# Performance work log

Hardware: AMD Instinct MI355X
Metric: run time of the kernel (lower is better)

## Reference

```python
import jax, jax.numpy as jnp
import numpy as np

EPS = 1e-12

def _l2norm(v):
    return v / (jnp.linalg.norm(v) + EPS)

def _spectral_norm_weight(W, u):
    # torch spectral_norm with n_power_iterations=1: v = norm(W^T u); u' = norm(W v);
    # sigma = u'^T W v with u', v detached; returns W / sigma.
    v = jax.lax.stop_gradient(_l2norm(W.T @ u))
    u2 = jax.lax.stop_gradient(_l2norm(W @ v))
    sigma = u2 @ (W @ v)
    return W / sigma

def setup_inputs() -> dict:
    key = jax.random.key(0)
    ks = jax.random.split(key, 8)
    C, H, W = 64, 96, 96
    Cfg = C // 8
    g = 1e-2  # small weight scale (module uses orthogonal init with tiny gain)
    return {
        "x":  jax.random.normal(ks[0], (1, C, H, W), jnp.float32),
        "Wf": jax.random.normal(ks[1], (Cfg, C), jnp.float32) * g,
        "bf": jnp.zeros((Cfg,), jnp.float32),
        "Wg": jax.random.normal(ks[2], (Cfg, C), jnp.float32) * g,
        "bg": jnp.zeros((Cfg,), jnp.float32),
        "Wh": jax.random.normal(ks[3], (C, C), jnp.float32) * g,
        "bh": jnp.zeros((C,), jnp.float32),
        "gamma": jax.random.normal(ks[4], (1,), jnp.float32),
        "uf": jax.random.normal(ks[5], (Cfg,), jnp.float32),
        "ug": jax.random.normal(ks[6], (Cfg,), jnp.float32),
        "uh": jax.random.normal(ks[7], (C,), jnp.float32),
    }

def reference(x, Wf, bf, Wg, bg, Wh, bh, gamma, uf, ug, uh):
    B, C, H, Wd = x.shape
    N = H * Wd
    xf = x.reshape(B, C, N)  # 1x1 convs act per-pixel -> matmul over channel dim
    Wf_sn = _spectral_norm_weight(Wf, uf)
    Wg_sn = _spectral_norm_weight(Wg, ug)
    Wh_sn = _spectral_norm_weight(Wh, uh)
    f_flat = jnp.einsum('oc,bcn->bon', Wf_sn, xf) + bf[:, None]  # [B,Cfg,N]
    g_flat = jnp.einsum('oc,bcn->bon', Wg_sn, xf) + bg[:, None]  # [B,Cfg,N]
    h_flat = jnp.einsum('oc,bcn->bon', Wh_sn, xf) + bh[:, None]  # [B,C,N]
    # s[b,n,m] = sum_k g[b,k,n] * f[b,k,m]  (g^T f)
    s = jnp.einsum('bkn,bkm->bnm', g_flat, f_flat)  # [B,N,N]
    beta = jax.nn.softmax(s, axis=1)                # softmax over dim=1 (g axis)
    o = jnp.einsum('bcn,bnm->bcm', h_flat, beta)    # [B,C,N]
    o = o.reshape(B, C, H, Wd)
    return gamma * o + x
```

## Files before the change

kernel.cpp:

```cpp
#include <hip/hip_runtime.h>
#include <hip/hip_bf16.h>

#define NPIX 9216
#define MTILES (NPIX / 16)

typedef __attribute__((ext_vector_type(4))) float f32x4;
typedef __attribute__((ext_vector_type(8))) short bf16x8;
typedef __attribute__((ext_vector_type(2))) unsigned int u32x2;

__device__ __forceinline__ void gload_lds16(const void* g, void* l) {
  __builtin_amdgcn_global_load_lds(
      (const __attribute__((address_space(1))) unsigned int*)g,
      (__attribute__((address_space(3))) unsigned int*)l, 16, 0, 0);
}
__device__ __forceinline__ void gload_lds4(const void* g, void* l) {
  __builtin_amdgcn_global_load_lds(
      (const __attribute__((address_space(1))) unsigned int*)g,
      (__attribute__((address_space(3))) unsigned int*)l, 4, 0, 0);
}
#define LDS_OFF(p) ((unsigned)(unsigned long long)(const __attribute__((address_space(3))) char*)(const char*)(p))

__global__ __launch_bounds__(256) void spectral_kernel(
    const float* __restrict__ Wf, const float* __restrict__ bfv,
    const float* __restrict__ Wg, const float* __restrict__ bgv,
    const float* __restrict__ Wh, const float* __restrict__ bhv,
    const float* __restrict__ uf, const float* __restrict__ ug,
    const float* __restrict__ uh,
    float* __restrict__ Wsc, float* __restrict__ bsc) {
  __shared__ float vsh3[3][64];
  __shared__ float is_s[3];
  const int tid = threadIdx.x;
  const int wv = tid >> 6, t = tid & 63;
  if (wv < 3) {
    const float* W = (wv == 0) ? Wf : (wv == 1) ? Wg : Wh;
    const float* u = (wv == 0) ? uf : (wv == 1) ? ug : uh;
    const int O = (wv == 2) ? 64 : 8;
    float v = 0.f;
    for (int o = 0; o < O; ++o) v += W[o * 64 + t] * u[o];
    float s = v * v;
    for (int off = 32; off; off >>= 1) s += __shfl_xor(s, off);
    vsh3[wv][t] = v / (sqrtf(s) + 1e-12f);
    float wvv = 0.f;
    if (t < O) { for (int c = 0; c < 64; ++c) wvv += W[t * 64 + c] * vsh3[wv][c]; }
    float s2 = (t < O) ? wvv * wvv : 0.f;
    for (int off = 32; off; off >>= 1) s2 += __shfl_xor(s2, off);
    const float nw = sqrtf(s2);
    if (t == 0) is_s[wv] = (nw + 1e-12f) / s2;
  }
  __syncthreads();
  const float sf = is_s[0] * 0.25f, sg = is_s[1], sh = is_s[2];
  for (int e = tid; e < 5120; e += 256) {
    const int r = e >> 6, c = e & 63;
    float val;
    if (r < 8)       val = Wf[r * 64 + c] * sf;
    else if (r < 16) val = Wg[(r - 8) * 64 + c] * sg;
    else             val = Wh[(r - 16) * 64 + c] * sh;
    Wsc[e] = val;
  }
  if (tid < 80) {
    bsc[tid] = (tid < 8) ? bfv[tid] * 0.25f
             : (tid < 16) ? bgv[tid - 8] : bhv[tid - 16];
  }
}

__global__ __launch_bounds__(256) void fgh_kernel(
    const float* __restrict__ x,
    const float* __restrict__ Wsc, const float* __restrict__ bsc,
    ushort* __restrict__ Qp, ushort* __restrict__ Kp, ushort* __restrict__ Vt2) {
  const int tid = threadIdx.x;
  const int px = tid & 63;
  const int rw = __builtin_amdgcn_readfirstlane(tid >> 6);
  const int r0 = blockIdx.y * 16 + rw * 4;
  const int p  = blockIdx.x * 64 + px;

  float xv[64];
  #pragma unroll
  for (int c = 0; c < 64; ++c) xv[c] = x[c * NPIX + p];

  float acc0 = 0.f, acc1 = 0.f, acc2 = 0.f, acc3 = 0.f;
  const float* w0 = Wsc + (r0 + 0) * 64;
  const float* w1 = Wsc + (r0 + 1) * 64;
  const float* w2 = Wsc + (r0 + 2) * 64;
  const float* w3 = Wsc + (r0 + 3) * 64;
  #pragma unroll
  for (int c = 0; c < 64; ++c) {
    const float xc = xv[c];
    acc0 += w0[c] * xc; acc1 += w1[c] * xc;
    acc2 += w2[c] * xc; acc3 += w3[c] * xc;
  }

  const int tile = p >> 5, nt = p & 31;
  const int tt = nt >> 4, gg = (nt >> 2) & 3, ii = nt & 3;
  const int kbase = tile * 512 + nt * 8;
  float accs[4] = {acc0, acc1, acc2, acc3};
  #pragma unroll
  for (int j = 0; j < 4; ++j) {
    const int r = r0 + j;
    const float val = accs[j] + bsc[r];
    if (r < 8) {
      const __hip_bfloat16 h = __float2bfloat16(val);
      const float hf = __bfloat162float(h);
      const __hip_bfloat16 lo = __float2bfloat16(val - hf);
      Qp[p * 16 + r]     = *(const ushort*)&h;
      Qp[p * 16 + 8 + r] = *(const ushort*)&lo;
    } else if (r < 16) {
      const int rk = r - 8;
      const __hip_bfloat16 h = __float2bfloat16(val);
      const float hf = __bfloat162float(h);
      const __hip_bfloat16 lo = __float2bfloat16(val - hf);
      Kp[kbase + rk]       = *(const ushort*)&h;
      Kp[kbase + 256 + rk] = *(const ushort*)&lo;
    } else {
      const int rv = r - 16;
      const __hip_bfloat16 hv = __float2bfloat16(val);
      const int idx = tile * 2048 +
          ((rv * 32 + gg * 8 + tt * 4 + ii) ^ (((rv >> 1) & 7) << 3));
      Vt2[idx] = *(const ushort*)&hv;
    }
  }
}

template <int S>
__global__ __launch_bounds__(256) void attn_kernel(
    const ushort* __restrict__ Qp, const ushort* __restrict__ Kp,
    const ushort* __restrict__ Vt2,
    ushort* __restrict__ Om,
    float* __restrict__ Sm) {
  constexpr int NSEG = NPIX / S;
  constexpr int NT = NSEG / 32;
  __shared__ ushort Vs[4][2048];
  __shared__ ushort Ks[4][512];
  const int tid  = threadIdx.x;
  const int w    = tid >> 6;
  const int l    = tid & 63;
  const int mloc = l & 15;
  const int g    = l >> 4;
  const int spl  = blockIdx.y;
  const int mrow = blockIdx.x * 64 + w * 16 + mloc;

  bf16x8 qh = *(const bf16x8*)(Qp + mrow * 16);
  bf16x8 ql = *(const bf16x8*)(Qp + mrow * 16 + 8);
  asm volatile("" : "+v"(qh), "+v"(ql));

  const int n0 = spl * NSEG;
  const char* vsrc = (const char*)Vt2 + ((size_t)(n0 >> 5)) * 4096 + w * 1024 + l * 16;
  const char* ksrc = (const char*)Kp + ((size_t)(n0 >> 5)) * 1024 + w * 256 + l * 4;

  #define STAGE(t_) do {                                                  \
    const int b_ = (t_) & 3;                                              \
    gload_lds16(vsrc + (size_t)(t_) * 4096, (char*)&Vs[b_][0] + w * 1024);\
    gload_lds4 (ksrc + (size_t)(t_) * 1024, (char*)&Ks[b_][0] + w * 256); \
  } while (0)

  STAGE(0);
  STAGE(1);

  const unsigned ks_base = LDS_OFF(&Ks[0][0]);
  const unsigned vs_base = LDS_OFF(&Vs[0][0]);
  const unsigned vswz = (mloc * 64 + g * 16) ^ (((mloc >> 1) & 7) << 4);

  float mx = -INFINITY, ls = 0.f;
  const f32x4 zero = {0.f, 0.f, 0.f, 0.f};
  f32x4 acc0 = zero, acc1 = zero, acc2 = zero, acc3 = zero;

  for (int t = 0; t < NT; ++t) {
    const int b = t & 3;
    if (t + 2 < NT) {
      STAGE(t + 2);
      asm volatile("s_waitcnt vmcnt(4)" ::: "memory");
    } else if (t + 1 < NT) {
      asm volatile("s_waitcnt vmcnt(2)" ::: "memory");
    } else {
      asm volatile("s_waitcnt vmcnt(0)" ::: "memory");
    }
    __builtin_amdgcn_s_barrier();

    const unsigned kaddr = ks_base + b * 1024 + mloc * 16;
    const unsigned vaddr = vs_base + b * 4096 + vswz;
    bf16x8 kh0, kl0, kh1, kl1, v0, v1, v2, v3;
    asm volatile("ds_read_b128 %0, %1"            : "=v"(kh0) : "v"(kaddr));
    asm volatile("ds_read_b128 %0, %1 offset:256" : "=v"(kh1) : "v"(kaddr));
    asm volatile("ds_read_b128 %0, %1 offset:512" : "=v"(kl0) : "v"(kaddr));
    asm volatile("ds_read_b128 %0, %1 offset:768" : "=v"(kl1) : "v"(kaddr));
    asm volatile("ds_read_b128 %0, %1"            : "=v"(v0)  : "v"(vaddr));
    asm volatile("ds_read_b128 %0, %1 offset:1024": "=v"(v1)  : "v"(vaddr));
    asm volatile("ds_read_b128 %0, %1 offset:2048": "=v"(v2)  : "v"(vaddr));
    asm volatile("ds_read_b128 %0, %1 offset:3072": "=v"(v3)  : "v"(vaddr));
    asm volatile("s_waitcnt lgkmcnt(0)" ::: "memory");
    __builtin_amdgcn_sched_barrier(0);

    f32x4 s0 = zero, s1 = zero;
    s0 = __builtin_amdgcn_mfma_f32_16x16x32_bf16(kh0, qh, s0, 0, 0, 0);
    s1 = __builtin_amdgcn_mfma_f32_16x16x32_bf16(kh1, qh, s1, 0, 0, 0);
    s0 = __builtin_amdgcn_mfma_f32_16x16x32_bf16(kh0, ql, s0, 0, 0, 0);
    s1 = __builtin_amdgcn_mfma_f32_16x16x32_bf16(kh1, ql, s1, 0, 0, 0);
    s0 = __builtin_amdgcn_mfma_f32_16x16x32_bf16(kl0, qh, s0, 0, 0, 0);
    s1 = __builtin_amdgcn_mfma_f32_16x16x32_bf16(kl1, qh, s1, 0, 0, 0);

    const float tm = fmaxf(
        fmaxf(fmaxf(s0[0], s0[1]), fmaxf(s0[2], s0[3])),
        fmaxf(fmaxf(s1[0], s1[1]), fmaxf(s1[2], s1[3])));
    if (__any(tm > mx + 8.0f)) {
      float tr = fmaxf(tm, __shfl_xor(tm, 16));
      tr = fmaxf(tr, __shfl_xor(tr, 32));
      const float mxn = fmaxf(mx, tr);
      const float corr = __expf(mx - mxn);
      ls *= corr;
      const float c0 = __shfl(corr, (g << 2) + 0);
      const float c1 = __shfl(corr, (g << 2) + 1);
      const float c2 = __shfl(corr, (g << 2) + 2);
      const float c3 = __shfl(corr, (g << 2) + 3);
      acc0[0] *= c0; acc0[1] *= c1; acc0[2] *= c2; acc0[3] *= c3;
      acc1[0] *= c0; acc1[1] *= c1; acc1[2] *= c2; acc1[3] *= c3;
      acc2[0] *= c0; acc2[1] *= c1; acc2[2] *= c2; acc2[3] *= c3;
      acc3[0] *= c0; acc3[1] *= c1; acc3[2] *= c2; acc3[3] *= c3;
      mx = mxn;
    }
    float pj[8];
    pj[0] = __expf(s0[0] - mx); pj[1] = __expf(s0[1] - mx);
    pj[2] = __expf(s0[2] - mx); pj[3] = __expf(s0[3] - mx);
    pj[4] = __expf(s1[0] - mx); pj[5] = __expf(s1[1] - mx);
    pj[6] = __expf(s1[2] - mx); pj[7] = __expf(s1[3] - mx);
    ls += ((pj[0] + pj[1]) + (pj[2] + pj[3])) + ((pj[4] + pj[5]) + (pj[6] + pj[7]));

    union { unsigned int u[4]; bf16x8 v; } pu;
    #pragma unroll
    for (int jj = 0; jj < 4; ++jj) {
      unsigned int r;
      asm("v_cvt_pk_bf16_f32 %0, %1, %2" : "=v"(r) : "v"(pj[2 * jj]), "v"(pj[2 * jj + 1]));
      pu.u[jj] = r;
    }
    acc0 = __builtin_amdgcn_mfma_f32_16x16x32_bf16(pu.v, v0, acc0, 0, 0, 0);
    acc1 = __builtin_amdgcn_mfma_f32_16x16x32_bf16(pu.v, v1, acc1, 0, 0, 0);
    acc2 = __builtin_amdgcn_mfma_f32_16x16x32_bf16(pu.v, v2, acc2, 0, 0, 0);
    acc3 = __builtin_amdgcn_mfma_f32_16x16x32_bf16(pu.v, v3, acc3, 0, 0, 0);
  }
  #undef STAGE

  ls += __shfl_xor(ls, 16);
  ls += __shfl_xor(ls, 32);

  const size_t mt = (size_t)blockIdx.x * 4 + w;
  ushort* Ob = Om + (mt * S + spl) * 1024;
  float*  Sb = Sm + (mt * S + spl) * 32;
  #pragma unroll
  for (int ct = 0; ct < 4; ++ct) {
    const f32x4 a = (ct == 0) ? acc0 : (ct == 1) ? acc1 : (ct == 2) ? acc2 : acc3;
    unsigned int r0, r1;
    asm("v_cvt_pk_bf16_f32 %0, %1, %2" : "=v"(r0) : "v"(a[0]), "v"(a[1]));
    asm("v_cvt_pk_bf16_f32 %0, %1, %2" : "=v"(r1) : "v"(a[2]), "v"(a[3]));
    u32x2 pk; pk[0] = r0; pk[1] = r1;
    *(u32x2*)(Ob + (ct * 16 + mloc) * 16 + 4 * g) = pk;
  }
  if (l < 16) { Sb[l] = mx; Sb[16 + l] = ls; }
}

template <int S>
__global__ __launch_bounds__(256) void combine_kernel(
    const ushort* __restrict__ Om, const float* __restrict__ Sm,
    const float* __restrict__ x, const float* __restrict__ gammap,
    float* __restrict__ out) {
  const int mt = blockIdx.x;
  const int m0 = mt * 16;
  const float gamma = gammap[0];
  const float* Sb = Sm + (size_t)mt * S * 32;
  const ushort* Ob = Om + (size_t)mt * S * 1024;
  for (int e = threadIdx.x; e < 1024; e += 256) {
    const int m = e & 15, c = e >> 4;
    float M = -INFINITY;
    #pragma unroll
    for (int s = 0; s < S; ++s) M = fmaxf(M, Sb[s * 32 + m]);
    float L = 0.f, val = 0.f;
    #pragma unroll
    for (int s = 0; s < S; ++s) {
      const float wgt = __expf(Sb[s * 32 + m] - M);
      L += Sb[s * 32 + 16 + m] * wgt;
      union { unsigned int i; float f; } cv;
      cv.i = ((unsigned int)Ob[s * 1024 + e]) << 16;
      val += cv.f * wgt;
    }
    const int idx = c * NPIX + m0 + m;
    out[idx] = gamma * (val / L) + x[idx];
  }
}

extern "C" void kernel_launch(void* const* d_in, const int* in_sizes, int n_in,
                              void* d_out, int out_size, void* d_ws, size_t ws_size,
                              hipStream_t stream) {
  const float* x     = (const float*)d_in[0];
  const float* Wf    = (const float*)d_in[1];
  const float* bf    = (const float*)d_in[2];
  const float* Wg    = (const float*)d_in[3];
  const float* bg    = (const float*)d_in[4];
  const float* Wh    = (const float*)d_in[5];
  const float* bh    = (const float*)d_in[6];
  const float* gamma = (const float*)d_in[7];
  const float* uf    = (const float*)d_in[8];
  const float* ug    = (const float*)d_in[9];
  const float* uh    = (const float*)d_in[10];
  float* out = (float*)d_out;

  char* ws = (char*)d_ws;
  float*  Wsc = (float*)(ws);
  float*  bsc = (float*)(ws + 20480);
  ushort* Qp  = (ushort*)(ws + 21504);
  ushort* Kp  = (ushort*)(ws + 21504 + NPIX * 16 * 2);
  ushort* Vt2 = (ushort*)(ws + 21504 + 2 * NPIX * 16 * 2);
  const size_t off = 21504 + (size_t)2 * NPIX * 16 * 2 + (size_t)NPIX * 64 * 2;
  ushort* Om = (ushort*)(ws + off);
  const size_t need16 = off + (size_t)MTILES * 16 * 1024 * 2 + (size_t)MTILES * 16 * 32 * 4;

  spectral_kernel<<<1, 256, 0, stream>>>(Wf, bf, Wg, bg, Wh, bh, uf, ug, uh, Wsc, bsc);
  fgh_kernel<<<dim3(NPIX / 64, 5), 256, 0, stream>>>(x, Wsc, bsc, Qp, Kp, Vt2);
  if (ws_size >= need16) {
    float* Sm = (float*)(ws + off + (size_t)MTILES * 16 * 1024 * 2);
    attn_kernel<16><<<dim3(NPIX / 64, 16), 256, 0, stream>>>(Qp, Kp, Vt2, Om, Sm);
    combine_kernel<16><<<MTILES, 256, 0, stream>>>(Om, Sm, x, gamma, out);
  } else {
    float* Sm = (float*)(ws + off + (size_t)MTILES * 8 * 1024 * 2);
    attn_kernel<8><<<dim3(NPIX / 64, 8), 256, 0, stream>>>(Qp, Kp, Vt2, Om, Sm);
    combine_kernel<8><<<MTILES, 256, 0, stream>>>(Om, Sm, x, gamma, out);
  }
}
```

Baseline: 77.60 us.

## Restructure attention pipeline: 2-wave blocks, triple buffering, exp2 softmax, split 8

Attention blocks shrink from four waves to two, covering 32 query rows, and the KV split is fixed at 8, so the grid becomes 288x8 with 128 threads per block. Staging moves from a 4-deep to a 3-deep LDS ring and is issued after the barrier, using only 16-byte global-to-LDS loads. The log2(e) factor is folded into the f-projection weights and bias so every softmax exp becomes exp2f, with the rescale threshold adjusted to match. The V LDS reads are waited on only just before the PV MFMAs, letting them overlap the QK MFMAs and exponentials. Fewer waves per block and more blocks change occupancy and per-block LDS reuse, and the fallback path for small workspaces is removed.

```diff
diff --git a/kernel.cpp b/kernel.cpp
--- a/kernel.cpp
+++ b/kernel.cpp
@@ -3,6 +3,7 @@
 
 #define NPIX 9216
 #define MTILES (NPIX / 16)
+#define SPLIT 8
 
 typedef __attribute__((ext_vector_type(4))) float f32x4;
 typedef __attribute__((ext_vector_type(8))) short bf16x8;
@@ -12,11 +13,6 @@
   __builtin_amdgcn_global_load_lds(
       (const __attribute__((address_space(1))) unsigned int*)g,
       (__attribute__((address_space(3))) unsigned int*)l, 16, 0, 0);
-}
-__device__ __forceinline__ void gload_lds4(const void* g, void* l) {
-  __builtin_amdgcn_global_load_lds(
-      (const __attribute__((address_space(1))) unsigned int*)g,
-      (__attribute__((address_space(3))) unsigned int*)l, 4, 0, 0);
 }
 #define LDS_OFF(p) ((unsigned)(unsigned long long)(const __attribute__((address_space(3))) char*)(const char*)(p))
 
@@ -48,7 +44,8 @@
     if (t == 0) is_s[wv] = (nw + 1e-12f) / s2;
   }
   __syncthreads();
-  const float sf = is_s[0] * 0.25f, sg = is_s[1], sh = is_s[2];
+  const float LOG2E = 1.44269504f;
+  const float sf = is_s[0] * 0.25f * LOG2E, sg = is_s[1], sh = is_s[2];
   for (int e = tid; e < 5120; e += 256) {
     const int r = e >> 6, c = e & 63;
     float val;
@@ -58,7 +55,7 @@
     Wsc[e] = val;
   }
   if (tid < 80) {
-    bsc[tid] = (tid < 8) ? bfv[tid] * 0.25f
+    bsc[tid] = (tid < 8) ? bfv[tid] * 0.25f * LOG2E
              : (tid < 16) ? bgv[tid - 8] : bhv[tid - 16];
   }
 }
@@ -121,35 +118,36 @@
 }
 
 template <int S>
-__global__ __launch_bounds__(256) void attn_kernel(
+__global__ __launch_bounds__(128) void attn_kernel(
     const ushort* __restrict__ Qp, const ushort* __restrict__ Kp,
     const ushort* __restrict__ Vt2,
     ushort* __restrict__ Om,
     float* __restrict__ Sm) {
   constexpr int NSEG = NPIX / S;
   constexpr int NT = NSEG / 32;
-  __shared__ ushort Vs[4][2048];
-  __shared__ ushort Ks[4][512];
+  __shared__ ushort Vs[3][2048];
+  __shared__ ushort Ks[3][512];
   const int tid  = threadIdx.x;
   const int w    = tid >> 6;
   const int l    = tid & 63;
   const int mloc = l & 15;
   const int g    = l >> 4;
   const int spl  = blockIdx.y;
-  const int mrow = blockIdx.x * 64 + w * 16 + mloc;
+  const int mrow = blockIdx.x * 32 + w * 16 + mloc;
 
   bf16x8 qh = *(const bf16x8*)(Qp + mrow * 16);
   bf16x8 ql = *(const bf16x8*)(Qp + mrow * 16 + 8);
   asm volatile("" : "+v"(qh), "+v"(ql));
 
   const int n0 = spl * NSEG;
-  const char* vsrc = (const char*)Vt2 + ((size_t)(n0 >> 5)) * 4096 + w * 1024 + l * 16;
-  const char* ksrc = (const char*)Kp + ((size_t)(n0 >> 5)) * 1024 + w * 256 + l * 4;
-
-  #define STAGE(t_) do {                                                  \
-    const int b_ = (t_) & 3;                                              \
-    gload_lds16(vsrc + (size_t)(t_) * 4096, (char*)&Vs[b_][0] + w * 1024);\
-    gload_lds4 (ksrc + (size_t)(t_) * 1024, (char*)&Ks[b_][0] + w * 256); \
+  const char* vsrc = (const char*)Vt2 + ((size_t)(n0 >> 5)) * 4096 + w * 2048 + l * 16;
+  const char* ksrc = (const char*)Kp + ((size_t)(n0 >> 5)) * 1024 + l * 16;
+
+  #define STAGE(t_) do {                                                      \
+    const int b_ = (t_) % 3;                                                  \
+    gload_lds16(vsrc + (size_t)(t_) * 4096,        (char*)&Vs[b_][0] + w * 2048);        \
+    gload_lds16(vsrc + (size_t)(t_) * 4096 + 1024, (char*)&Vs[b_][0] + w * 2048 + 1024); \
+    gload_lds16(ksrc + (size_t)(t_) * 1024,        (char*)&Ks[b_][0]);        \
   } while (0)
 
   STAGE(0);
@@ -163,17 +161,16 @@
   const f32x4 zero = {0.f, 0.f, 0.f, 0.f};
   f32x4 acc0 = zero, acc1 = zero, acc2 = zero, acc3 = zero;
 
+  #pragma unroll 6
   for (int t = 0; t < NT; ++t) {
-    const int b = t & 3;
-    if (t + 2 < NT) {
-      STAGE(t + 2);
-      asm volatile("s_waitcnt vmcnt(4)" ::: "memory");
-    } else if (t + 1 < NT) {
-      asm volatile("s_waitcnt vmcnt(2)" ::: "memory");
+    const int b = t % 3;
+    if (t + 1 < NT) {
+      asm volatile("s_waitcnt vmcnt(3)" ::: "memory");
     } else {
       asm volatile("s_waitcnt vmcnt(0)" ::: "memory");
     }
     __builtin_amdgcn_s_barrier();
+    if (t + 2 < NT) STAGE(t + 2);
 
     const unsigned kaddr = ks_base + b * 1024 + mloc * 16;
     const unsigned vaddr = vs_base + b * 4096 + vswz;
@@ -186,7 +183,7 @@
     asm volatile("ds_read_b128 %0, %1 offset:1024": "=v"(v1)  : "v"(vaddr));
     asm volatile("ds_read_b128 %0, %1 offset:2048": "=v"(v2)  : "v"(vaddr));
     asm volatile("ds_read_b128 %0, %1 offset:3072": "=v"(v3)  : "v"(vaddr));
-    asm volatile("s_waitcnt lgkmcnt(0)" ::: "memory");
+    asm volatile("s_waitcnt lgkmcnt(4)" ::: "memory");
     __builtin_amdgcn_sched_barrier(0);
 
     f32x4 s0 = zero, s1 = zero;
@@ -197,14 +194,15 @@
     s0 = __builtin_amdgcn_mfma_f32_16x16x32_bf16(kl0, qh, s0, 0, 0, 0);
     s1 = __builtin_amdgcn_mfma_f32_16x16x32_bf16(kl1, qh, s1, 0, 0, 0);
 
-    const float tm = fmaxf(
-        fmaxf(fmaxf(s0[0], s0[1]), fmaxf(s0[2], s0[3])),
-        fmaxf(fmaxf(s1[0], s1[1]), fmaxf(s1[2], s1[3])));
-    if (__any(tm > mx + 8.0f)) {
+    const float m1 = fmaxf(fmaxf(s0[0], s0[1]), s0[2]);
+    const float m2 = fmaxf(fmaxf(s0[3], s1[0]), s1[1]);
+    const float m3 = fmaxf(fmaxf(s1[2], s1[3]), m1);
+    const float tm = fmaxf(m2, m3);
+    if (__any(tm > mx + 11.5416f)) {
       float tr = fmaxf(tm, __shfl_xor(tm, 16));
       tr = fmaxf(tr, __shfl_xor(tr, 32));
       const float mxn = fmaxf(mx, tr);
-      const float corr = __expf(mx - mxn);
+      const float corr = exp2f(mx - mxn);
       ls *= corr;
       const float c0 = __shfl(corr, (g << 2) + 0);
       const float c1 = __shfl(corr, (g << 2) + 1);
@@ -217,10 +215,10 @@
       mx = mxn;
     }
     float pj[8];
-    pj[0] = __expf(s0[0] - mx); pj[1] = __expf(s0[1] - mx);
-    pj[2] = __expf(s0[2] - mx); pj[3] = __expf(s0[3] - mx);
-    pj[4] = __expf(s1[0] - mx); pj[5] = __expf(s1[1] - mx);
-    pj[6] = __expf(s1[2] - mx); pj[7] = __expf(s1[3] - mx);
+    pj[0] = exp2f(s0[0] - mx); pj[1] = exp2f(s0[1] - mx);
+    pj[2] = exp2f(s0[2] - mx); pj[3] = exp2f(s0[3] - mx);
+    pj[4] = exp2f(s1[0] - mx); pj[5] = exp2f(s1[1] - mx);
+    pj[6] = exp2f(s1[2] - mx); pj[7] = exp2f(s1[3] - mx);
     ls += ((pj[0] + pj[1]) + (pj[2] + pj[3])) + ((pj[4] + pj[5]) + (pj[6] + pj[7]));
 
     union { unsigned int u[4]; bf16x8 v; } pu;
@@ -230,6 +228,8 @@
       asm("v_cvt_pk_bf16_f32 %0, %1, %2" : "=v"(r) : "v"(pj[2 * jj]), "v"(pj[2 * jj + 1]));
       pu.u[jj] = r;
     }
+    asm volatile("s_waitcnt lgkmcnt(0)" ::: "memory");
+    __builtin_amdgcn_sched_barrier(0);
     acc0 = __builtin_amdgcn_mfma_f32_16x16x32_bf16(pu.v, v0, acc0, 0, 0, 0);
     acc1 = __builtin_amdgcn_mfma_f32_16x16x32_bf16(pu.v, v1, acc1, 0, 0, 0);
     acc2 = __builtin_amdgcn_mfma_f32_16x16x32_bf16(pu.v, v2, acc2, 0, 0, 0);
@@ -240,7 +240,7 @@
   ls += __shfl_xor(ls, 16);
   ls += __shfl_xor(ls, 32);
 
-  const size_t mt = (size_t)blockIdx.x * 4 + w;
+  const size_t mt = (size_t)blockIdx.x * 2 + w;
   ushort* Ob = Om + (mt * S + spl) * 1024;
   float*  Sb = Sm + (mt * S + spl) * 32;
   #pragma unroll
@@ -273,7 +273,7 @@
     float L = 0.f, val = 0.f;
     #pragma unroll
     for (int s = 0; s < S; ++s) {
-      const float wgt = __expf(Sb[s * 32 + m] - M);
+      const float wgt = exp2f(Sb[s * 32 + m] - M);
       L += Sb[s * 32 + 16 + m] * wgt;
       union { unsigned int i; float f; } cv;
       cv.i = ((unsigned int)Ob[s * 1024 + e]) << 16;
@@ -308,17 +308,10 @@
   ushort* Vt2 = (ushort*)(ws + 21504 + 2 * NPIX * 16 * 2);
   const size_t off = 21504 + (size_t)2 * NPIX * 16 * 2 + (size_t)NPIX * 64 * 2;
   ushort* Om = (ushort*)(ws + off);
-  const size_t need16 = off + (size_t)MTILES * 16 * 1024 * 2 + (size_t)MTILES * 16 * 32 * 4;
+  float*  Sm = (float*)(ws + off + (size_t)MTILES * SPLIT * 1024 * 2);
 
   spectral_kernel<<<1, 256, 0, stream>>>(Wf, bf, Wg, bg, Wh, bh, uf, ug, uh, Wsc, bsc);
   fgh_kernel<<<dim3(NPIX / 64, 5), 256, 0, stream>>>(x, Wsc, bsc, Qp, Kp, Vt2);
-  if (ws_size >= need16) {
-    float* Sm = (float*)(ws + off + (size_t)MTILES * 16 * 1024 * 2);
-    attn_kernel<16><<<dim3(NPIX / 64, 16), 256, 0, stream>>>(Qp, Kp, Vt2, Om, Sm);
-    combine_kernel<16><<<MTILES, 256, 0, stream>>>(Om, Sm, x, gamma, out);
-  } else {
-    float* Sm = (float*)(ws + off + (size_t)MTILES * 8 * 1024 * 2);
-    attn_kernel<8><<<dim3(NPIX / 64, 8), 256, 0, stream>>>(Qp, Kp, Vt2, Om, Sm);
-    combine_kernel<8><<<MTILES, 256, 0, stream>>>(Om, Sm, x, gamma, out);
-  }
-}
+  attn_kernel<SPLIT><<<dim3(NPIX / 32, SPLIT), 128, 0, stream>>>(Qp, Kp, Vt2, Om, Sm);
+  combine_kernel<SPLIT><<<MTILES, 256, 0, stream>>>(Om, Sm, x, gamma, out);
+}
```

Result: slower. 83.02 us (+7.0%).

## Process two query tiles per wave, fold log2e into Q, split combine blocks

Applied to the files above, without the earlier changes.

Each attention wave now handles two 16-row query tiles, so every K/V tile staged in LDS is reused twice and the grid is halved. QK MFMAs start after a partial LDS wait, overlapping with the V reads. Log2(e) is folded into the f weights and bias so the softmax can use exp2f, with the rescale threshold adjusted to match. The combine kernel is split into four blocks per tile for more parallelism. The cost is roughly double the accumulator registers, which may lower occupancy, plus fewer attention blocks.

```diff
diff --git a/kernel.cpp b/kernel.cpp
--- a/kernel.cpp
+++ b/kernel.cpp
@@ -48,7 +48,8 @@
     if (t == 0) is_s[wv] = (nw + 1e-12f) / s2;
   }
   __syncthreads();
-  const float sf = is_s[0] * 0.25f, sg = is_s[1], sh = is_s[2];
+  const float LOG2E = 1.44269504f;
+  const float sf = is_s[0] * 0.25f * LOG2E, sg = is_s[1], sh = is_s[2];
   for (int e = tid; e < 5120; e += 256) {
     const int r = e >> 6, c = e & 63;
     float val;
@@ -58,7 +59,7 @@
     Wsc[e] = val;
   }
   if (tid < 80) {
-    bsc[tid] = (tid < 8) ? bfv[tid] * 0.25f
+    bsc[tid] = (tid < 8) ? bfv[tid] * 0.25f * LOG2E
              : (tid < 16) ? bgv[tid - 8] : bhv[tid - 16];
   }
 }
@@ -120,6 +121,45 @@
   }
 }
 
+__device__ __forceinline__ void softmax_step(
+    const f32x4 s0, const f32x4 s1, int g, float& mx, float& ls,
+    f32x4& a0, f32x4& a1, f32x4& a2, f32x4& a3, bf16x8& pv) {
+  const float m1 = fmaxf(fmaxf(s0[0], s0[1]), s0[2]);
+  const float m2 = fmaxf(fmaxf(s0[3], s1[0]), s1[1]);
+  const float m3 = fmaxf(fmaxf(s1[2], s1[3]), m1);
+  const float tm = fmaxf(m2, m3);
+  if (__any(tm > mx + 11.5416f)) {
+    float tr = fmaxf(tm, __shfl_xor(tm, 16));
+    tr = fmaxf(tr, __shfl_xor(tr, 32));
+    const float mxn = fmaxf(mx, tr);
+    const float corr = exp2f(mx - mxn);
+    ls *= corr;
+    const float c0 = __shfl(corr, (g << 2) + 0);
+    const float c1 = __shfl(corr, (g << 2) + 1);
+    const float c2 = __shfl(corr, (g << 2) + 2);
+    const float c3 = __shfl(corr, (g << 2) + 3);
+    a0[0] *= c0; a0[1] *= c1; a0[2] *= c2; a0[3] *= c3;
+    a1[0] *= c0; a1[1] *= c1; a1[2] *= c2; a1[3] *= c3;
+    a2[0] *= c0; a2[1] *= c1; a2[2] *= c2; a2[3] *= c3;
+    a3[0] *= c0; a3[1] *= c1; a3[2] *= c2; a3[3] *= c3;
+    mx = mxn;
+  }
+  float pj[8];
+  pj[0] = exp2f(s0[0] - mx); pj[1] = exp2f(s0[1] - mx);
+  pj[2] = exp2f(s0[2] - mx); pj[3] = exp2f(s0[3] - mx);
+  pj[4] = exp2f(s1[0] - mx); pj[5] = exp2f(s1[1] - mx);
+  pj[6] = exp2f(s1[2] - mx); pj[7] = exp2f(s1[3] - mx);
+  ls += ((pj[0] + pj[1]) + (pj[2] + pj[3])) + ((pj[4] + pj[5]) + (pj[6] + pj[7]));
+  union { unsigned int u[4]; bf16x8 v; } pu;
+  #pragma unroll
+  for (int jj = 0; jj < 4; ++jj) {
+    unsigned int r;
+    asm("v_cvt_pk_bf16_f32 %0, %1, %2" : "=v"(r) : "v"(pj[2 * jj]), "v"(pj[2 * jj + 1]));
+    pu.u[jj] = r;
+  }
+  pv = pu.v;
+}
+
 template <int S>
 __global__ __launch_bounds__(256) void attn_kernel(
     const ushort* __restrict__ Qp, const ushort* __restrict__ Kp,
@@ -136,11 +176,14 @@
   const int mloc = l & 15;
   const int g    = l >> 4;
   const int spl  = blockIdx.y;
-  const int mrow = blockIdx.x * 64 + w * 16 + mloc;
-
-  bf16x8 qh = *(const bf16x8*)(Qp + mrow * 16);
-  bf16x8 ql = *(const bf16x8*)(Qp + mrow * 16 + 8);
-  asm volatile("" : "+v"(qh), "+v"(ql));
+  const int mrow0 = blockIdx.x * 128 + w * 32 + mloc;
+  const int mrow1 = mrow0 + 16;
+
+  bf16x8 qh0 = *(const bf16x8*)(Qp + mrow0 * 16);
+  bf16x8 ql0 = *(const bf16x8*)(Qp + mrow0 * 16 + 8);
+  bf16x8 qh1 = *(const bf16x8*)(Qp + mrow1 * 16);
+  bf16x8 ql1 = *(const bf16x8*)(Qp + mrow1 * 16 + 8);
+  asm volatile("" : "+v"(qh0), "+v"(ql0), "+v"(qh1), "+v"(ql1));
 
   const int n0 = spl * NSEG;
   const char* vsrc = (const char*)Vt2 + ((size_t)(n0 >> 5)) * 4096 + w * 1024 + l * 16;
@@ -159,9 +202,10 @@
   const unsigned vs_base = LDS_OFF(&Vs[0][0]);
   const unsigned vswz = (mloc * 64 + g * 16) ^ (((mloc >> 1) & 7) << 4);
 
-  float mx = -INFINITY, ls = 0.f;
+  float mx0 = -INFINITY, ls0 = 0.f, mx1 = -INFINITY, ls1 = 0.f;
   const f32x4 zero = {0.f, 0.f, 0.f, 0.f};
-  f32x4 acc0 = zero, acc1 = zero, acc2 = zero, acc3 = zero;
+  f32x4 p0a0 = zero, p0a1 = zero, p0a2 = zero, p0a3 = zero;
+  f32x4 p1a0 = zero, p1a1 = zero, p1a2 = zero, p1a3 = zero;
 
   for (int t = 0; t < NT; ++t) {
     const int b = t & 3;
@@ -186,73 +230,66 @@
     asm volatile("ds_read_b128 %0, %1 offset:1024": "=v"(v1)  : "v"(vaddr));
     asm volatile("ds_read_b128 %0, %1 offset:2048": "=v"(v2)  : "v"(vaddr));
     asm volatile("ds_read_b128 %0, %1 offset:3072": "=v"(v3)  : "v"(vaddr));
+    asm volatile("s_waitcnt lgkmcnt(4)" ::: "memory");
+    __builtin_amdgcn_sched_barrier(0);
+
+    f32x4 s00 = zero, s01 = zero, s10 = zero, s11 = zero;
+    s00 = __builtin_amdgcn_mfma_f32_16x16x32_bf16(kh0, qh0, s00, 0, 0, 0);
+    s01 = __builtin_amdgcn_mfma_f32_16x16x32_bf16(kh1, qh0, s01, 0, 0, 0);
+    s10 = __builtin_amdgcn_mfma_f32_16x16x32_bf16(kh0, qh1, s10, 0, 0, 0);
+    s11 = __builtin_amdgcn_mfma_f32_16x16x32_bf16(kh1, qh1, s11, 0, 0, 0);
+    s00 = __builtin_amdgcn_mfma_f32_16x16x32_bf16(kh0, ql0, s00, 0, 0, 0);
+    s01 = __builtin_amdgcn_mfma_f32_16x16x32_bf16(kh1, ql0, s01, 0, 0, 0);
+    s10 = __builtin_amdgcn_mfma_f32_16x16x32_bf16(kh0, ql1, s10, 0, 0, 0);
+    s11 = __builtin_amdgcn_mfma_f32_16x16x32_bf16(kh1, ql1, s11, 0, 0, 0);
+    s00 = __builtin_amdgcn_mfma_f32_16x16x32_bf16(kl0, qh0, s00, 0, 0, 0);
+    s01 = __builtin_amdgcn_mfma_f32_16x16x32_bf16(kl1, qh0, s01, 0, 0, 0);
+    s10 = __builtin_amdgcn_mfma_f32_16x16x32_bf16(kl0, qh1, s10, 0, 0, 0);
+    s11 = __builtin_amdgcn_mfma_f32_16x16x32_bf16(kl1, qh1, s11, 0, 0, 0);
+
+    bf16x8 pv0, pv1;
+    softmax_step(s00, s01, g, mx0, ls0, p0a0, p0a1, p0a2, p0a3, pv0);
+    softmax_step(s10, s11, g, mx1, ls1, p1a0, p1a1, p1a2, p1a3, pv1);
+
     asm volatile("s_waitcnt lgkmcnt(0)" ::: "memory");
     __builtin_amdgcn_sched_barrier(0);
-
-    f32x4 s0 = zero, s1 = zero;
-    s0 = __builtin_amdgcn_mfma_f32_16x16x32_bf16(kh0, qh, s0, 0, 0, 0);
-    s1 = __builtin_amdgcn_mfma_f32_16x16x32_bf16(kh1, qh, s1, 0, 0, 0);
-    s0 = __builtin_amdgcn_mfma_f32_16x16x32_bf16(kh0, ql, s0, 0, 0, 0);
-    s1 = __builtin_amdgcn_mfma_f32_16x16x32_bf16(kh1, ql, s1, 0, 0, 0);
-    s0 = __builtin_amdgcn_mfma_f32_16x16x32_bf16(kl0, qh, s0, 0, 0, 0);
-    s1 = __builtin_amdgcn_mfma_f32_16x16x32_bf16(kl1, qh, s1, 0, 0, 0);
-
-    const float tm = fmaxf(
-        fmaxf(fmaxf(s0[0], s0[1]), fmaxf(s0[2], s0[3])),
-        fmaxf(fmaxf(s1[0], s1[1]), fmaxf(s1[2], s1[3])));
-    if (__any(tm > mx + 8.0f)) {
-      float tr = fmaxf(tm, __shfl_xor(tm, 16));
-      tr = fmaxf(tr, __shfl_xor(tr, 32));
-      const float mxn = fmaxf(mx, tr);
-      const float corr = __expf(mx - mxn);
-      ls *= corr;
-      const float c0 = __shfl(corr, (g << 2) + 0);
-      const float c1 = __shfl(corr, (g << 2) + 1);
-      const float c2 = __shfl(corr, (g << 2) + 2);
-      const float c3 = __shfl(corr, (g << 2) + 3);
-      acc0[0] *= c0; acc0[1] *= c1; acc0[2] *= c2; acc0[3] *= c3;
-      acc1[0] *= c0; acc1[1] *= c1; acc1[2] *= c2; acc1[3] *= c3;
-      acc2[0] *= c0; acc2[1] *= c1; acc2[2] *= c2; acc2[3] *= c3;
-      acc3[0] *= c0; acc3[1] *= c1; acc3[2] *= c2; acc3[3] *= c3;
-      mx = mxn;
-    }
-    float pj[8];
-    pj[0] = __expf(s0[0] - mx); pj[1] = __expf(s0[1] - mx);
-    pj[2] = __expf(s0[2] - mx); pj[3] = __expf(s0[3] - mx);
-    pj[4] = __expf(s1[0] - mx); pj[5] = __expf(s1[1] - mx);
-    pj[6] = __expf(s1[2] - mx); pj[7] = __expf(s1[3] - mx);
-    ls += ((pj[0] + pj[1]) + (pj[2] + pj[3])) + ((pj[4] + pj[5]) + (pj[6] + pj[7]));
-
-    union { unsigned int u[4]; bf16x8 v; } pu;
-    #pragma unroll
-    for (int jj = 0; jj < 4; ++jj) {
-      unsigned int r;
-      asm("v_cvt_pk_bf16_f32 %0, %1, %2" : "=v"(r) : "v"(pj[2 * jj]), "v"(pj[2 * jj + 1]));
-      pu.u[jj] = r;
-    }
-    acc0 = __builtin_amdgcn_mfma_f32_16x16x32_bf16(pu.v, v0, acc0, 0, 0, 0);
-    acc1 = __builtin_amdgcn_mfma_f32_16x16x32_bf16(pu.v, v1, acc1, 0, 0, 0);
-    acc2 = __builtin_amdgcn_mfma_f32_16x16x32_bf16(pu.v, v2, acc2, 0, 0, 0);
-    acc3 = __builtin_amdgcn_mfma_f32_16x16x32_bf16(pu.v, v3, acc3, 0, 0, 0);
+    p0a0 = __builtin_amdgcn_mfma_f32_16x16x32_bf16(pv0, v0, p0a0, 0, 0, 0);
+    p1a0 = __builtin_amdgcn_mfma_f32_16x16x32_bf16(pv1, v0, p1a0, 0, 0, 0);
+    p0a1 = __builtin_amdgcn_mfma_f32_16x16x32_bf16(pv0, v1, p0a1, 0, 0, 0);
+    p1a1 = __builtin_amdgcn_mfma_f32_16x16x32_bf16(pv1, v1, p1a1, 0, 0, 0);
+    p0a2 = __builtin_amdgcn_mfma_f32_16x16x32_bf16(pv0, v2, p0a2, 0, 0, 0);
+    p1a2 = __builtin_amdgcn_mfma_f32_16x16x32_bf16(pv1, v2, p1a2, 0, 0, 0);
+    p0a3 = __builtin_amdgcn_mfma_f32_16x16x32_bf16(pv0, v3, p0a3, 0, 0, 0);
+    p1a3 = __builtin_amdgcn_mfma_f32_16x16x32_bf16(pv1, v3, p1a3, 0, 0, 0);
   }
   #undef STAGE
 
-  ls += __shfl_xor(ls, 16);
-  ls += __shfl_xor(ls, 32);
-
-  const size_t mt = (size_t)blockIdx.x * 4 + w;
-  ushort* Ob = Om + (mt * S + spl) * 1024;
-  float*  Sb = Sm + (mt * S + spl) * 32;
+  ls0 += __shfl_xor(ls0, 16); ls0 += __shfl_xor(ls0, 32);
+  ls1 += __shfl_xor(ls1, 16); ls1 += __shfl_xor(ls1, 32);
+
+  const size_t mt0 = (size_t)blockIdx.x * 8 + w * 2;
+  ushort* Ob0 = Om + (mt0 * S + spl) * 1024;
+  ushort* Ob1 = Om + ((mt0 + 1) * S + spl) * 1024;
+  float*  Sb0 = Sm + (mt0 * S + spl) * 32;
+  float*  Sb1 = Sm + ((mt0 + 1) * S + spl) * 32;
   #pragma unroll
   for (int ct = 0; ct < 4; ++ct) {
-    const f32x4 a = (ct == 0) ? acc0 : (ct == 1) ? acc1 : (ct == 2) ? acc2 : acc3;
-    unsigned int r0, r1;
+    const f32x4 a = (ct == 0) ? p0a0 : (ct == 1) ? p0a1 : (ct == 2) ? p0a2 : p0a3;
+    const f32x4 c = (ct == 0) ? p1a0 : (ct == 1) ? p1a1 : (ct == 2) ? p1a2 : p1a3;
+    unsigned int r0, r1, r2, r3;
     asm("v_cvt_pk_bf16_f32 %0, %1, %2" : "=v"(r0) : "v"(a[0]), "v"(a[1]));
     asm("v_cvt_pk_bf16_f32 %0, %1, %2" : "=v"(r1) : "v"(a[2]), "v"(a[3]));
-    u32x2 pk; pk[0] = r0; pk[1] = r1;
-    *(u32x2*)(Ob + (ct * 16 + mloc) * 16 + 4 * g) = pk;
-  }
-  if (l < 16) { Sb[l] = mx; Sb[16 + l] = ls; }
+    asm("v_cvt_pk_bf16_f32 %0, %1, %2" : "=v"(r2) : "v"(c[0]), "v"(c[1]));
+    asm("v_cvt_pk_bf16_f32 %0, %1, %2" : "=v"(r3) : "v"(c[2]), "v"(c[3]));
+    u32x2 pk0; pk0[0] = r0; pk0[1] = r1;
+    u32x2 pk1; pk1[0] = r2; pk1[1] = r3;
+    *(u32x2*)(Ob0 + (ct * 16 + mloc) * 16 + 4 * g) = pk0;
+    *(u32x2*)(Ob1 + (ct * 16 + mloc) * 16 + 4 * g) = pk1;
+  }
+  if (l < 16) {
+    Sb0[l] = mx0; Sb0[16 + l] = ls0;
+    Sb1[l] = mx1; Sb1[16 + l] = ls1;
+  }
 }
 
 template <int S>
@@ -260,28 +297,27 @@
     const ushort* __restrict__ Om, const float* __restrict__ Sm,
     const float* __restrict__ x, const float* __restrict__ gammap,
     float* __restrict__ out) {
-  const int mt = blockIdx.x;
+  const int mt = blockIdx.x >> 2;
   const int m0 = mt * 16;
+  const int e  = (blockIdx.x & 3) * 256 + threadIdx.x;
   const float gamma = gammap[0];
   const float* Sb = Sm + (size_t)mt * S * 32;
   const ushort* Ob = Om + (size_t)mt * S * 1024;
-  for (int e = threadIdx.x; e < 1024; e += 256) {
-    const int m = e & 15, c = e >> 4;
-    float M = -INFINITY;
-    #pragma unroll
-    for (int s = 0; s < S; ++s) M = fmaxf(M, Sb[s * 32 + m]);
-    float L = 0.f, val = 0.f;
-    #pragma unroll
-    for (int s = 0; s < S; ++s) {
-      const float wgt = __expf(Sb[s * 32 + m] - M);
-      L += Sb[s * 32 + 16 + m] * wgt;
-      union { unsigned int i; float f; } cv;
-      cv.i = ((unsigned int)Ob[s * 1024 + e]) << 16;
-      val += cv.f * wgt;
-    }
-    const int idx = c * NPIX + m0 + m;
-    out[idx] = gamma * (val / L) + x[idx];
-  }
+  const int m = e & 15, c = e >> 4;
+  float M = -INFINITY;
+  #pragma unroll
+  for (int s = 0; s < S; ++s) M = fmaxf(M, Sb[s * 32 + m]);
+  float L = 0.f, val = 0.f;
+  #pragma unroll
+  for (int s = 0; s < S; ++s) {
+    const float wgt = exp2f(Sb[s * 32 + m] - M);
+    L += Sb[s * 32 + 16 + m] * wgt;
+    union { unsigned int i; float f; } cv;
+    cv.i = ((unsigned int)Ob[s * 1024 + e]) << 16;
+    val += cv.f * wgt;
+  }
+  const int idx = c * NPIX + m0 + m;
+  out[idx] = gamma * (val / L) + x[idx];
 }
 
 extern "C" void kernel_launch(void* const* d_in, const int* in_sizes, int n_in,
@@ -314,11 +350,11 @@
   fgh_kernel<<<dim3(NPIX / 64, 5), 256, 0, stream>>>(x, Wsc, bsc, Qp, Kp, Vt2);
   if (ws_size >= need16) {
     float* Sm = (float*)(ws + off + (size_t)MTILES * 16 * 1024 * 2);
-    attn_kernel<16><<<dim3(NPIX / 64, 16), 256, 0, stream>>>(Qp, Kp, Vt2, Om, Sm);
-    combine_kernel<16><<<MTILES, 256, 0, stream>>>(Om, Sm, x, gamma, out);
+    attn_kernel<16><<<dim3(NPIX / 128, 16), 256, 0, stream>>>(Qp, Kp, Vt2, Om, Sm);
+    combine_kernel<16><<<MTILES * 4, 256, 0, stream>>>(Om, Sm, x, gamma, out);
   } else {
     float* Sm = (float*)(ws + off + (size_t)MTILES * 8 * 1024 * 2);
-    attn_kernel<8><<<dim3(NPIX / 64, 8), 256, 0, stream>>>(Qp, Kp, Vt2, Om, Sm);
-    combine_kernel<8><<<MTILES, 256, 0, stream>>>(Om, Sm, x, gamma, out);
-  }
-}
+    attn_kernel<8><<<dim3(NPIX / 128, 8), 256, 0, stream>>>(Qp, Kp, Vt2, Om, Sm);
+    combine_kernel<8><<<MTILES * 4, 256, 0, stream>>>(Om, Sm, x, gamma, out);
+  }
+}
```

Result: slower. 87.12 us (+12.3%).
